# Kernel optimization log

Measured on AMD Instinct MI355X. Metric: run time of the kernel, lower is better.

Reference implementation:

```python
import jax, jax.numpy as jnp
import numpy as np

HEADS = 4
EPS_LN = 1e-6
EPS_IN = 1e-5


def _ln(x, g, b):
    m = x.mean(-1, keepdims=True)
    v = ((x - m) ** 2).mean(-1, keepdims=True)
    return (x - m) / jnp.sqrt(v + EPS_LN) * g + b


def _inorm(s):
    # nn.InstanceNorm2d(1) (affine=False): normalize each (batch, channel=head)
    # slice over the last two (N, N) dims, biased variance, eps=1e-5.
    m = s.mean((-2, -1), keepdims=True)
    v = ((s - m) ** 2).mean((-2, -1), keepdims=True)
    return (s - m) / jnp.sqrt(v + EPS_IN)


def setup_inputs() -> dict:
    key = jax.random.key(0)
    ks = jax.random.split(key, 32)
    B, C, Hh = 8, 256, HEADS
    sc = 1.0 / np.sqrt(C)

    def n(k, shape, s):
        return jax.random.normal(k, shape, jnp.float32) * s

    return {
        "x": n(ks[0], (B, C, 6, 6, 6), 1.0),
        # global branch params
        "g_tok_w": n(ks[1], (C,), 0.05), "g_tok_b": jnp.zeros((C,), jnp.float32),
        "g_ln1_g": jnp.ones((C,), jnp.float32), "g_ln1_b": jnp.zeros((C,), jnp.float32),
        "g_wq": n(ks[2], (C, C * Hh), sc), "g_wk": n(ks[3], (C, C * Hh), sc),
        "g_wv": n(ks[4], (C, C * Hh), sc), "g_wo": n(ks[5], (C * Hh, C), sc),
        "g_ln2_g": jnp.ones((C,), jnp.float32), "g_ln2_b": jnp.zeros((C,), jnp.float32),
        "g_mo_w": n(ks[6], (C, C), sc), "g_mo_b": jnp.zeros((C,), jnp.float32),
        # local branch params
        "l_pw": n(ks[7], (8, 8), 0.35), "l_pb": jnp.zeros((8,), jnp.float32),
        "l_ln1_g": jnp.ones((C,), jnp.float32), "l_ln1_b": jnp.zeros((C,), jnp.float32),
        "l_wq": n(ks[8], (C, C * Hh), sc), "l_wk": n(ks[9], (C, C * Hh), sc),
        "l_wv": n(ks[10], (C, C * Hh), sc), "l_wo": n(ks[11], (C * Hh, C), sc),
        "l_ln2_g": jnp.ones((C,), jnp.float32), "l_ln2_b": jnp.zeros((C,), jnp.float32),
        "l_mo_w": n(ks[12], (C, C), sc), "l_mo_b": jnp.zeros((C,), jnp.float32),
    }


def _global_branch(x, tok_w, tok_b, ln1_g, ln1_b, wq, wk, wv, wo, ln2_g, ln2_b, mo_w, mo_b):
    B, C, D, H, W = x.shape
    Hh = HEADS
    # TokenLearner_Global: conv1x1x1 (1->256) then mean over (D,H,W), then
    # view(B,C,C).mean(dim=1).  Since the conv is 1x1 on a single input channel,
    # this collapses exactly to: w * mean(x over C,D,H,W) + b.
    m = x.mean((1, 2, 3, 4))                       # (B,)
    tok = m[:, None] * tok_w + tok_b               # (B, C)
    res = tok
    t = _ln(tok, ln1_g, ln1_b)                     # (B, C)
    q = (t @ wq).reshape(B, Hh, C)                 # heads outer in the 1024 split
    k = (t @ wk).reshape(B, Hh, C)
    v = (t @ wv).reshape(B, Hh, C)
    # mh_q^T (B,h,C,1) @ mh_k (B,h,1,C) -> rank-1 (B,h,C,C) score map
    score = q[:, :, :, None] * k[:, :, None, :]
    a = jax.nn.softmax(_inorm(score), axis=-1)
    o = jnp.einsum('bhij,bhj->bhi', a, v)          # attn @ mh_v^T -> (B,h,C)
    # permute(0,3,2,1).view: flatten as (c, heads) with c outer
    o = o.transpose(0, 2, 1).reshape(B, C * Hh)
    out = o @ wo                                   # (B, C)
    tok2 = _ln(out + res, ln2_g, ln2_b)            # (B, C)
    # map_out conv1x1 + GELU on a spatially-constant expand -> compute once
    g = jax.nn.gelu(jnp.einsum('bc,oc->bo', tok2, mo_w) + mo_b, approximate=False)
    return jnp.broadcast_to(g[:, :, None, None, None], (B, C, D, H, W))


def _local_branch(x, pw, pb, ln1_g, ln1_b, wq, wk, wv, wo, ln2_g, ln2_b, mo_w, mo_b):
    B, C, D, H, W = x.shape
    Hh = HEADS
    # TokenLearner_Local: conv3d(1->8, k=2, s=2) per channel == patchify 2x2x2
    xp = x.reshape(B * C, 3, 2, 3, 2, 3, 2).transpose(0, 1, 3, 5, 2, 4, 6)
    xp = xp.reshape(B * C, 27, 8)                  # (BC, patches, patch_vol)
    tok = xp @ pw.T + pb                           # (BC, 27, 8) embed_dim=8
    tok = tok.reshape(B, C, 3, 3, 3, 2, 2, 2)
    # res: (b c)(d h w)(p1 p2 p3) -> b (d p1 h p2 w p3) c
    res = tok.transpose(0, 2, 5, 3, 6, 4, 7, 1).reshape(B, 216, C)
    # attn input: (b c)(d h w)(p1 p2 p3) -> (b d h w) (p1 p2 p3) c
    e = tok.reshape(B, C, 3, 3, 3, 8).transpose(0, 2, 3, 4, 5, 1).reshape(B * 27, 8, C)
    e = _ln(e, ln1_g, ln1_b)
    # (c heads) split: c outer, heads inner
    q = (e @ wq).reshape(B * 27, 8, C, Hh).transpose(0, 3, 2, 1)   # (B27,h,C,8)
    k = (e @ wk).reshape(B * 27, 8, C, Hh).transpose(0, 3, 1, 2)   # (B27,h,8,C)
    v = (e @ wv).reshape(B * 27, 8, C, Hh).transpose(0, 3, 2, 1)   # (B27,h,C,8)
    score = q @ k                                                  # (B27,h,C,C)
    a = jax.nn.softmax(_inorm(score), axis=-1)
    o = a @ v                                                      # (B27,h,C,8)
    # (b d h w) heads c (p1 p2 p3) -> b (d p1 h p2 w p3) (c heads)
    o = o.reshape(B, 3, 3, 3, Hh, C, 2, 2, 2)
    o = o.transpose(0, 1, 6, 2, 7, 3, 8, 5, 4).reshape(B, 216, C * Hh)
    out = o @ wo                                                   # (B,216,C)
    t2 = _ln(out + res, ln2_g, ln2_b)
    xm = t2.transpose(0, 2, 1).reshape(B, C, D, H, W)
    return jax.nn.gelu(
        jnp.einsum('bcdhw,oc->bodhw', xm, mo_w) + mo_b[None, :, None, None, None],
        approximate=False)


def reference(x,
              g_tok_w, g_tok_b, g_ln1_g, g_ln1_b, g_wq, g_wk, g_wv, g_wo,
              g_ln2_g, g_ln2_b, g_mo_w, g_mo_b,
              l_pw, l_pb, l_ln1_g, l_ln1_b, l_wq, l_wk, l_wv, l_wo,
              l_ln2_g, l_ln2_b, l_mo_w, l_mo_b):
    g = _global_branch(x, g_tok_w, g_tok_b, g_ln1_g, g_ln1_b, g_wq, g_wk, g_wv,
                       g_wo, g_ln2_g, g_ln2_b, g_mo_w, g_mo_b)
    l = _local_branch(x, l_pw, l_pb, l_ln1_g, l_ln1_b, l_wq, l_wk, l_wv,
                      l_wo, l_ln2_g, l_ln2_b, l_mo_w, l_mo_b)
    return x + g + l
```

## Files before the change

### kernel.cpp

```cpp
#include <hip/hip_runtime.h>
#include <stdint.h>
#include <math.h>

#define DEVFN __device__ __forceinline__
typedef unsigned short u16;
typedef short bf16x8 __attribute__((ext_vector_type(8)));
typedef float f32x4  __attribute__((ext_vector_type(4)));

DEVFN float blk_sum(float v, float* s4) {
  #pragma unroll
  for (int o = 32; o > 0; o >>= 1) v += __shfl_down(v, o, 64);
  __syncthreads();
  if ((threadIdx.x & 63) == 0) s4[threadIdx.x >> 6] = v;
  __syncthreads();
  return s4[0] + s4[1] + s4[2] + s4[3];
}

DEVFN void blk_sum2(float a, float b, float* out, float (*s)[4]) {
  #pragma unroll
  for (int o = 32; o > 0; o >>= 1) {
    a += __shfl_down(a, o, 64);
    b += __shfl_down(b, o, 64);
  }
  __syncthreads();
  if ((threadIdx.x & 63) == 0) {
    int wi = threadIdx.x >> 6;
    s[0][wi] = a; s[1][wi] = b;
  }
  __syncthreads();
  out[0] = s[0][0] + s[0][1] + s[0][2] + s[0][3];
  out[1] = s[1][0] + s[1][1] + s[1][2] + s[1][3];
}

DEVFN void blk_sum17(float* v, float (*s)[4]) {
  #pragma unroll
  for (int o = 32; o > 0; o >>= 1)
    #pragma unroll
    for (int i = 0; i < 17; ++i) v[i] += __shfl_down(v[i], o, 64);
  __syncthreads();
  if ((threadIdx.x & 63) == 0) {
    int wi = threadIdx.x >> 6;
    #pragma unroll
    for (int i = 0; i < 17; ++i) s[i][wi] = v[i];
  }
  __syncthreads();
  #pragma unroll
  for (int i = 0; i < 17; ++i) v[i] = s[i][0] + s[i][1] + s[i][2] + s[i][3];
}

DEVFN float gelu_f(float x) {
  return 0.5f * x * (1.f + erff(x * 0.7071067811865475f));
}

DEVFN u16 bf16_rne(float f) {
  uint32_t u = __float_as_uint(f);
  return (u16)((u + 0x7fffu + ((u >> 16) & 1u)) >> 16);
}

DEVFN float bf2f(u16 v) { return __uint_as_float(((uint32_t)v) << 16); }

DEVFN void gload16(const u16* g, u16* l) {
  auto gp = (const __attribute__((address_space(1))) uint32_t*)(uintptr_t)g;
  auto lp = (__attribute__((address_space(3))) uint32_t*)(uintptr_t)l;
  __builtin_amdgcn_global_load_lds(gp, lp, 16, 0, 0);
}

DEVFN void stage64x256(const u16* G, size_t gstride, u16* L, int w, int lane) {
  #pragma unroll
  for (int i = 0; i < 8; ++i) {
    int row = w * 16 + 2 * i + (lane >> 5);
    int c16 = (lane & 31) ^ (row & 7);
    gload16(G + (size_t)row * gstride + c16 * 8, L + (w * 16 + 2 * i) * 256);
  }
}
DEVFN bf16x8 lread(const u16* L, int row, int k16) {
  return *(const bf16x8*)&L[row * 256 + ((k16 ^ (row & 7)) << 3)];
}

DEVFN void trc_tile(const float* __restrict__ in, u16* __restrict__ out,
                    int R, int C, int r0, int c0, float (*tile)[33], int tid) {
  int tx = tid & 31, ty = tid >> 5;
  for (int i = ty; i < 32; i += 8) tile[i][tx] = in[(size_t)(r0 + i) * C + c0 + tx];
  __syncthreads();
  for (int i = ty; i < 32; i += 8)
    out[(size_t)(c0 + i) * R + r0 + tx] = bf16_rne(tile[tx][i]);
}

__global__ __launch_bounds__(256) void k_l_tok_prep(
    const float* __restrict__ x, const float* __restrict__ pw,
    const float* __restrict__ pb, const float* __restrict__ g1,
    const float* __restrict__ b1, float* __restrict__ res,
    u16* __restrict__ eln_bf, float* __restrict__ g_part,
    const float* __restrict__ wq, const float* __restrict__ wk,
    const float* __restrict__ wv, const float* __restrict__ wo,
    const float* __restrict__ mow, u16* __restrict__ WcatT,
    u16* __restrict__ woT, u16* __restrict__ moB) {
  __shared__ __align__(16) char smem[8448];
  int bid0 = blockIdx.x, tid = threadIdx.x;
  if (bid0 < 216) {
    float* pws = (float*)smem;
    float (*s17)[4] = (float(*)[4])(smem + 256);
    int b = bid0 / 27, patch = bid0 % 27;
    int pz = patch / 9, py = (patch / 3) % 3, px = patch % 3;
    int c = tid;
    if (c < 64) pws[c] = pw[c];
    __syncthreads();
    const float* xb = x + (size_t)(b * 256 + c) * 216 + (2 * pz) * 36 + (2 * py) * 6 + 2 * px;
    float2 t00 = *(const float2*)&xb[0],  t01 = *(const float2*)&xb[6];
    float2 t10 = *(const float2*)&xb[36], t11 = *(const float2*)&xb[42];
    float xv[8] = {t00.x, t00.y, t01.x, t01.y, t10.x, t10.y, t11.x, t11.y};
    float v[8];
    #pragma unroll
    for (int p = 0; p < 8; ++p) {
      float a = pb[p];
      #pragma unroll
      for (int j = 0; j < 8; ++j) a = fmaf(xv[j], pws[p * 8 + j], a);
      v[p] = a;
    }
    float sums[17];
    sums[0] = xv[0] + xv[1] + xv[2] + xv[3] + xv[4] + xv[5] + xv[6] + xv[7];
    #pragma unroll
    for (int p = 0; p < 8; ++p) { sums[1 + p] = v[p]; sums[9 + p] = v[p] * v[p]; }
    blk_sum17(sums, s17);
    if (c == 0) g_part[bid0] = sums[0];
    float gg = g1[c], bb = b1[c];
    #pragma unroll
    for (int p = 0; p < 8; ++p) {
      int sz = 2 * pz + (p >> 2), sy = 2 * py + ((p >> 1) & 1), sx = 2 * px + (p & 1);
      int t = b * 216 + sz * 36 + sy * 6 + sx;
      float mu = sums[1 + p] * (1.f / 256.f);
      float var = sums[9 + p] * (1.f / 256.f) - mu * mu;
      res[t * 256 + c] = v[p];
      eln_bf[t * 256 + c] = bf16_rne((v[p] - mu) * rsqrtf(var + 1e-6f) * gg + bb);
    }
  } else {
    float (*tile)[33] = (float(*)[33])smem;
    int bid = bid0 - 216;
    if (bid < 768) {
      int which = bid >> 8, b2 = bid & 255;
      const float* in = (which == 0) ? wq : (which == 1) ? wk : wv;
      u16* out = WcatT + which * 262144;
      int r0 = (b2 & 7) * 32, c0 = (b2 >> 3) * 32;
      trc_tile(in, out, 256, 1024, r0, c0, tile, tid);
    } else if (bid < 1024) {
      int b2 = bid - 768;
      int r0 = (b2 & 31) * 32, c0 = (b2 >> 5) * 32;
      trc_tile(wo, woT, 1024, 256, r0, c0, tile, tid);
    } else {
      int i = (bid - 1024) * 256 + tid;
      moB[i] = bf16_rne(mow[i]);
    }
  }
}

__global__ __launch_bounds__(256) void k_gemm_qkv_fused(
    const u16* __restrict__ A, const u16* __restrict__ BT, u16* __restrict__ C,
    const float* __restrict__ g_part, const float* __restrict__ tw_,
    const float* __restrict__ tb_, const float* __restrict__ g1,
    const float* __restrict__ b1, const float* __restrict__ wq,
    const float* __restrict__ wk, const float* __restrict__ wv,
    float* __restrict__ gqkv) {
  __shared__ __align__(16) char smem[65536];
  int bid = blockIdx.x, tid = threadIdx.x;
  if (bid < 48) {
    float* ts = (float*)smem;
    float (*red)[4][8] = (float(*)[4][8])(smem + 8192);
    float* s4 = (float*)(smem + 16384);
    float* m_s = (float*)(smem + 16400);
    float tw = tw_[tid], tb = tb_[tid], gg = g1[tid], bb = b1[tid];
    float S1 = blk_sum(tw, s4);
    float S2 = blk_sum(tw * tw, s4);
    float S3 = blk_sum(tb, s4);
    float S4 = blk_sum(tb * tb, s4);
    float S5 = blk_sum(tw * tb, s4);
    {
      int b = tid >> 5, sl = tid & 31;
      float a = (sl < 27) ? g_part[b * 27 + sl] : 0.f;
      #pragma unroll
      for (int o = 16; o > 0; o >>= 1) a += __shfl_down(a, o, 32);
      if (sl == 0) m_s[b] = a * (1.f / 55296.f);
    }
    __syncthreads();
    #pragma unroll
    for (int b = 0; b < 8; ++b) {
      float m = m_s[b];
      float mu = (m * S1 + S3) * (1.f / 256.f);
      float var = (m * m * S2 + 2.f * m * S5 + S4) * (1.f / 256.f) - mu * mu;
      ts[b * 256 + tid] = (m * tw + tb - mu) * rsqrtf(var + 1e-6f) * gg + bb;
    }
    __syncthreads();
    int col0 = bid * 64;
    int cl = tid & 63, kq = tid >> 6;
    int col = col0 + cl;
    int m = col >> 10, cc = col & 1023;
    const float* W = (m == 0) ? wq : (m == 1) ? wk : wv;
    float acc[8] = {};
    for (int c0 = kq * 64; c0 < kq * 64 + 64; c0 += 8) {
      float wbuf[8];
      #pragma unroll
      for (int j = 0; j < 8; ++j) wbuf[j] = W[(c0 + j) * 1024 + cc];
      #pragma unroll
      for (int j = 0; j < 8; ++j) {
        float w = wbuf[j];
        #pragma unroll
        for (int b = 0; b < 8; ++b) acc[b] = fmaf(ts[b * 256 + c0 + j], w, acc[b]);
      }
    }
    #pragma unroll
    for (int b = 0; b < 8; ++b) red[cl][kq][b] = acc[b];
    __syncthreads();
    if (kq == 0) {
      #pragma unroll
      for (int b = 0; b < 8; ++b)
        gqkv[b * 3072 + col] = red[cl][0][b] + red[cl][1][b] + red[cl][2][b] + red[cl][3][b];
    }
  } else {
    const int N = 3072, K = 256;
    u16* aL = (u16*)smem;
    u16* bL = (u16*)smem + 16384;
    int t0 = bid - 48;
    int tile = (t0 & 7) * 162 + (t0 >> 3);
    int rowblk = (tile % 27) * 64, colblk = (tile / 27) * 64;
    int lane = tid & 63, w = tid >> 6;
    int wr = (w >> 1) * 32, wc = (w & 1) * 32;
    int fm = lane & 15, lg = lane >> 4;
    #pragma unroll
    for (int i = 0; i < 8; ++i) {
      int c16 = w * 8 + i;
      gload16(&A[(size_t)(rowblk + lane) * K + c16 * 8], aL + c16 * 512);
      gload16(&BT[(size_t)(colblk + lane) * K + c16 * 8], bL + c16 * 512);
    }
    __syncthreads();
    f32x4 acc[2][2] = {};
    #pragma unroll
    for (int kk = 0; kk < 8; ++kk) {
      int k16 = kk * 4 + lg;
      bf16x8 bn0 = *(const bf16x8*)&bL[k16 * 512 + (wc + fm) * 8];
      bf16x8 bn1 = *(const bf16x8*)&bL[k16 * 512 + (wc + 16 + fm) * 8];
      bf16x8 af0 = *(const bf16x8*)&aL[k16 * 512 + (wr + fm) * 8];
      bf16x8 af1 = *(const bf16x8*)&aL[k16 * 512 + (wr + 16 + fm) * 8];
      acc[0][0] = __builtin_amdgcn_mfma_f32_16x16x32_bf16(af0, bn0, acc[0][0], 0, 0, 0);
      acc[0][1] = __builtin_amdgcn_mfma_f32_16x16x32_bf16(af0, bn1, acc[0][1], 0, 0, 0);
      acc[1][0] = __builtin_amdgcn_mfma_f32_16x16x32_bf16(af1, bn0, acc[1][0], 0, 0, 0);
      acc[1][1] = __builtin_amdgcn_mfma_f32_16x16x32_bf16(af1, bn1, acc[1][1], 0, 0, 0);
    }
    __syncthreads();
    u16* ct = aL;
    #pragma unroll
    for (int mi = 0; mi < 2; ++mi)
      #pragma unroll
      for (int ni = 0; ni < 2; ++ni)
        #pragma unroll
        for (int r = 0; r < 4; ++r)
          ct[(wr + mi * 16 + lg * 4 + r) * 72 + wc + ni * 16 + fm] = bf16_rne(acc[mi][ni][r]);
    __syncthreads();
    #pragma unroll
    for (int pass = 0; pass < 2; ++pass) {
      int id = pass * 256 + tid;
      int r = id >> 3, u = id & 7;
      *(uint4*)&C[(size_t)(rowblk + r) * N + colblk + u * 8] = *(uint4*)&ct[r * 72 + u * 8];
    }
  }
}

__global__ __launch_bounds__(256) void k_l_attn_fused(
    const u16* __restrict__ qkv, u16* __restrict__ o_buf,
    const float* __restrict__ gq, float* __restrict__ g_o) {
  __shared__ __align__(16) uint4 Qb[256], Kb[256];
  __shared__ __align__(16) u16 vt[16][264];
  __shared__ __align__(16) u16 Pl[256][72];
  __shared__ float rqA[64][4], rkA[64][4], rlq[64][4], rlk[64][4], s_ab[2];
  int bid = blockIdx.x, tid = threadIdx.x;
  if (bid < 32) {
    float* ks = (float*)Qb;
    float* vs = ks + 256;
    float* s4 = (float*)Kb;
    int b = bid >> 2, h = bid & 3;
    int i = tid;
    const float* base = gq + b * 3072 + h * 256;
    float q = base[i];
    float k = base[1024 + i];
    ks[i] = k;
    vs[i] = base[2048 + i];
    float sq  = blk_sum(q, s4);
    float sq2 = blk_sum(q * q, s4);
    float sk  = blk_sum(k, s4);
    float sk2 = blk_sum(k * k, s4);
    float tot  = sq * sk * (1.f / 65536.f);
    float tot2 = sq2 * sk2 * (1.f / 65536.f);
    float rstd = rsqrtf(tot2 - tot * tot + 1e-5f);
    float A = rstd, B = -tot * rstd;
    float den = 0.f, num = 0.f;
    for (int j = 0; j < 256; ++j) {
      float w = __expf(fmaf(q * ks[j], A, B));
      den += w; num += w * vs[j];
    }
    g_o[b * 1024 + (i << 2) + h] = num / den;
    return;
  }
  int nb = bid - 32;
  int n = nb >> 2, h = nb & 3;
  int b = n / 27, patch = n % 27;
  int bz = 2 * (patch / 9), by = 2 * ((patch / 3) % 3), bx = 2 * (patch % 3);
  {
    int c = tid;
    u16 qv[8], kv[8], vv[8];
    #pragma unroll
    for (int p = 0; p < 8; ++p) {
      int t_l = b * 216 + (bz + (p >> 2)) * 36 + (by + ((p >> 1) & 1)) * 6 + (bx + (p & 1));
      const u16* row = qkv + (size_t)t_l * 3072 + (c << 2) + h;
      qv[p] = row[0]; kv[p] = row[1024]; vv[p] = row[2048];
    }
    uint32_t qw[4], kw[4];
    #pragma unroll
    for (int i = 0; i < 4; ++i) {
      qw[i] = (uint32_t)qv[2 * i] | ((uint32_t)qv[2 * i + 1] << 16);
      kw[i] = (uint32_t)kv[2 * i] | ((uint32_t)kv[2 * i + 1] << 16);
    }
    Qb[c] = make_uint4(qw[0], qw[1], qw[2], qw[3]);
    Kb[c] = make_uint4(kw[0], kw[1], kw[2], kw[3]);
    #pragma unroll
    for (int p = 0; p < 8; ++p) vt[p][c] = vv[p];
    vt[8][c] = 0x3F80u;
    #pragma unroll
    for (int r2 = 9; r2 < 16; ++r2) vt[r2][c] = 0;
  }
  __syncthreads();
  {
    int p = tid & 63, chunk = tid >> 6;
    int d = p >> 3, e = p & 7;
    float aq = 0.f, ak = 0.f, lq = 0.f, lk = 0.f;
    for (int cc = chunk * 64; cc < chunk * 64 + 64; ++cc) {
      const u16* qr = (const u16*)&Qb[cc];
      const u16* kr = (const u16*)&Kb[cc];
      float qd = bf2f(qr[d]), qe = bf2f(qr[e]);
      float kd = bf2f(kr[d]), ke = bf2f(kr[e]);
      aq = fmaf(qd, qe, aq); ak = fmaf(kd, ke, ak);
      if (e == 0) { lq += qd; lk += kd; }
    }
    rqA[p][chunk] = aq; rkA[p][chunk] = ak; rlq[p][chunk] = lq; rlk[p][chunk] = lk;
    __syncthreads();
    if (tid < 64) {
      float gq2 = rqA[tid][0] + rqA[tid][1] + rqA[tid][2] + rqA[tid][3];
      float gk = rkA[tid][0] + rkA[tid][1] + rkA[tid][2] + rkA[tid][3];
      float vprod = gq2 * gk, vmu = 0.f;
      if ((tid & 7) == 0) {
        float slq = rlq[tid][0] + rlq[tid][1] + rlq[tid][2] + rlq[tid][3];
        float slk = rlk[tid][0] + rlk[tid][1] + rlk[tid][2] + rlk[tid][3];
        vmu = slq * slk;
      }
      #pragma unroll
      for (int o = 32; o > 0; o >>= 1) {
        vprod += __shfl_down(vprod, o, 64);
        vmu   += __shfl_down(vmu, o, 64);
      }
      if (tid == 0) {
        float mu = vmu * (1.f / 65536.f), m2 = vprod * (1.f / 65536.f);
        float rstd = rsqrtf(m2 - mu * mu + 1e-5f);
        s_ab[0] = rstd; s_ab[1] = -mu * rstd;
      }
    }
    __syncthreads();
  }
  float Af = s_ab[0], Bf = s_ab[1];
  int lane = tid & 63, w = tid >> 6;
  int l15 = lane & 15, lg = lane >> 4;
  bf16x8 qf[4];
  #pragma unroll
  for (int qt = 0; qt < 4; ++qt)
    qf[qt] = *(const bf16x8*)&Qb[w * 64 + qt * 16 + l15];
  f32x4 acc_o[4] = {};
  #pragma unroll 1
  for (int jc = 0; jc < 4; ++jc) {
    bf16x8 kf[4];
    #pragma unroll
    for (int jt = 0; jt < 4; ++jt) {
      bf16x8 z = {};
      if (lg == 0) z = *(const bf16x8*)&Kb[jc * 64 + jt * 16 + l15];
      kf[jt] = z;
    }
    #pragma unroll
    for (int jt = 0; jt < 4; ++jt) {
      #pragma unroll
      for (int qt = 0; qt < 4; ++qt) {
        f32x4 zc = {};
        f32x4 s = __builtin_amdgcn_mfma_f32_16x16x32_bf16(kf[jt], qf[qt], zc, 0, 0, 0);
        float e0 = __expf(fmaf(s[0], Af, Bf));
        float e1 = __expf(fmaf(s[1], Af, Bf));
        float e2 = __expf(fmaf(s[2], Af, Bf));
        float e3 = __expf(fmaf(s[3], Af, Bf));
        uint32_t w0 = (__float_as_uint(e0) >> 16) | (__float_as_uint(e1) & 0xFFFF0000u);
        uint32_t w1 = (__float_as_uint(e2) >> 16) | (__float_as_uint(e3) & 0xFFFF0000u);
        int q = w * 64 + qt * 16 + l15;
        *(uint2*)&Pl[q][jt * 16 + lg * 4] = make_uint2(w0, w1);
      }
    }
    #pragma unroll
    for (int ks2 = 0; ks2 < 2; ++ks2) {
      bf16x8 vf = *(const bf16x8*)&vt[l15][jc * 64 + ks2 * 32 + lg * 8];
      #pragma unroll
      for (int qt = 0; qt < 4; ++qt) {
        bf16x8 pf = *(const bf16x8*)&Pl[w * 64 + qt * 16 + l15][ks2 * 32 + lg * 8];
        acc_o[qt] = __builtin_amdgcn_mfma_f32_16x16x32_bf16(pf, vf, acc_o[qt], 0, 0, 0);
      }
    }
  }
  int src = ((lane & 48) + 8) << 2;
  int p = l15;
  int t_l = b * 216 + (bz + (p >> 2)) * 36 + (by + ((p >> 1) & 1)) * 6 + (bx + (p & 1));
  #pragma unroll
  for (int qt = 0; qt < 4; ++qt) {
    #pragma unroll
    for (int r = 0; r < 4; ++r) {
      float den = __int_as_float(__builtin_amdgcn_ds_bpermute(src, __float_as_int(acc_o[qt][r])));
      if (p < 8) {
        int q = w * 64 + qt * 16 + lg * 4 + r;
        o_buf[(size_t)t_l * 1024 + (q << 2) + h] = bf16_rne(acc_o[qt][r] / den);
      }
    }
  }
}

__global__ __launch_bounds__(256) void k_gemm_sk_fused(
    const u16* __restrict__ A, const u16* __restrict__ BT, float* __restrict__ Cp,
    const float* __restrict__ g_o, const float* __restrict__ wo,
    float* __restrict__ part) {
  __shared__ __align__(16) char smem[65536];
  int bid = blockIdx.x, tid = threadIdx.x;
  if (bid < 32) {
    float* os = (float*)smem;
    int kc = bid;
    os[tid] = g_o[(tid >> 5) * 1024 + kc * 32 + (tid & 31)];
    __syncthreads();
    float acc[8] = {};
    #pragma unroll
    for (int kk = 0; kk < 32; ++kk) {
      float w = wo[(size_t)(kc * 32 + kk) * 256 + tid];
      #pragma unroll
      for (int b = 0; b < 8; ++b) acc[b] = fmaf(os[b * 32 + kk], w, acc[b]);
    }
    #pragma unroll
    for (int b = 0; b < 8; ++b) part[kc * 2048 + b * 256 + tid] = acc[b];
  } else {
    const int M = 1728, N = 256, K = 1024;
    u16* aL = (u16*)smem;
    u16* bL = (u16*)smem + 16384;
    int bid2 = bid - 32;
    int rowblk = (bid2 % 27) * 64, colblk = ((bid2 / 27) & 3) * 64;
    int kz = bid2 / 108;
    float* C = Cp + (size_t)kz * M * N;
    int lane = tid & 63, w = tid >> 6;
    int wr = (w >> 1) * 32, wc = (w & 1) * 32;
    int fm = lane & 15, lg = lane >> 4;
    f32x4 acc[2][2] = {};
    #pragma unroll 1
    for (int step = 0; step < 2; ++step) {
      int kt = kz * 512 + step * 256;
      __syncthreads();
      stage64x256(A + (size_t)rowblk * K + kt, K, aL, w, lane);
      stage64x256(BT + (size_t)colblk * K + kt, K, bL, w, lane);
      __syncthreads();
      #pragma unroll
      for (int kk = 0; kk < 8; ++kk) {
        int k16 = kk * 4 + lg;
        bf16x8 bn0 = lread(bL, wc + fm, k16);
        bf16x8 bn1 = lread(bL, wc + 16 + fm, k16);
        bf16x8 af0 = lread(aL, wr + fm, k16);
        bf16x8 af1 = lread(aL, wr + 16 + fm, k16);
        acc[0][0] = __builtin_amdgcn_mfma_f32_16x16x32_bf16(af0, bn0, acc[0][0], 0, 0, 0);
        acc[0][1] = __builtin_amdgcn_mfma_f32_16x16x32_bf16(af0, bn1, acc[0][1], 0, 0, 0);
        acc[1][0] = __builtin_amdgcn_mfma_f32_16x16x32_bf16(af1, bn0, acc[1][0], 0, 0, 0);
        acc[1][1] = __builtin_amdgcn_mfma_f32_16x16x32_bf16(af1, bn1, acc[1][1], 0, 0, 0);
      }
    }
    __syncthreads();
    float* ct = (float*)smem;
    #pragma unroll
    for (int mi = 0; mi < 2; ++mi)
      #pragma unroll
      for (int ni = 0; ni < 2; ++ni)
        #pragma unroll
        for (int r = 0; r < 4; ++r)
          ct[(wr + mi * 16 + lg * 4 + r) * 64 + wc + ni * 16 + fm] = acc[mi][ni][r];
    __syncthreads();
    #pragma unroll
    for (int pass = 0; pass < 4; ++pass) {
      int id = pass * 256 + tid;
      int r = id >> 4, u = id & 15;
      *(float4*)&C[(size_t)(rowblk + r) * N + colblk + u * 4] = *(float4*)&ct[r * 64 + u * 4];
    }
  }
}

__global__ __launch_bounds__(256) void k_l_ln2_fused(
    const float* __restrict__ proj0, const float* __restrict__ proj1,
    const float* __restrict__ res, const float* __restrict__ g2,
    const float* __restrict__ b2, u16* __restrict__ t2b,
    const float* __restrict__ part, const float* __restrict__ g_part,
    const float* __restrict__ tw_, const float* __restrict__ tb_,
    const float* __restrict__ gg2, const float* __restrict__ gb2,
    float* __restrict__ t2g) {
  __shared__ float s2v[2][4];
  int bid = blockIdx.x, c = threadIdx.x;
  if (bid < 8) {
    int b = bid;
    float a = (c < 27) ? g_part[b * 27 + c] : 0.f;
    float m = blk_sum(a, (float*)s2v) * (1.f / 55296.f);
    float v = m * tw_[c] + tb_[c];
    #pragma unroll
    for (int kc = 0; kc < 32; ++kc) v += part[kc * 2048 + b * 256 + c];
    float r2[2];
    blk_sum2(v, v * v, r2, s2v);
    float mu = r2[0] * (1.f / 256.f);
    float var = r2[1] * (1.f / 256.f) - mu * mu;
    t2g[b * 256 + c] = (v - mu) * rsqrtf(var + 1e-6f) * gg2[c] + gb2[c];
  } else {
    int t = bid - 8;
    float v = proj0[t * 256 + c] + proj1[t * 256 + c] + res[t * 256 + c];
    float r2[2];
    blk_sum2(v, v * v, r2, s2v);
    float mu = r2[0] * (1.f / 256.f);
    float var = r2[1] * (1.f / 256.f) - mu * mu;
    t2b[t * 256 + c] = bf16_rne((v - mu) * rsqrtf(var + 1e-6f) * g2[c] + b2[c]);
  }
}

__global__ __launch_bounds__(256) void k_g_mo(
    const float* __restrict__ t2g, const float* __restrict__ mow,
    const float* __restrict__ mob, float* __restrict__ g_vec) {
  __shared__ float ts[2048];
  int tid = threadIdx.x;
  for (int i = tid; i < 2048; i += 256) ts[i] = t2g[i];
  __syncthreads();
  int ol = tid >> 5, cs = tid & 31;
  int o = blockIdx.x * 8 + ol;
  const float* wrow = mow + (size_t)o * 256;
  float acc[8] = {};
  #pragma unroll
  for (int i = 0; i < 8; ++i) {
    float w = wrow[i * 32 + cs];
    #pragma unroll
    for (int b = 0; b < 8; ++b) acc[b] = fmaf(ts[b * 256 + i * 32 + cs], w, acc[b]);
  }
  #pragma unroll
  for (int b = 0; b < 8; ++b) {
    float v = acc[b];
    #pragma unroll
    for (int off = 16; off > 0; off >>= 1) v += __shfl_down(v, off, 32);
    if (cs == 0) g_vec[b * 256 + o] = gelu_f(v + mob[o]);
  }
}

__global__ __launch_bounds__(256) void k_gemm_mo_final(
    const u16* __restrict__ A, const u16* __restrict__ BT,
    const float* __restrict__ x, const float* __restrict__ gvec,
    const float* __restrict__ mob, float* __restrict__ out) {
  __shared__ __align__(16) char smem[65536];
  u16* aL = (u16*)smem;
  u16* bL = (u16*)smem + 16384;
  float (*ct)[65] = (float(*)[65])smem;
  const int K = 256;
  int tid = threadIdx.x;
  int rowblk = blockIdx.x * 64, colblk = blockIdx.y * 64;
  int lane = tid & 63, w = tid >> 6;
  int wr = (w >> 1) * 32, wc = (w & 1) * 32;
  int fm = lane & 15, lg = lane >> 4;
  stage64x256(A + (size_t)rowblk * K, K, aL, w, lane);
  stage64x256(BT + (size_t)colblk * K, K, bL, w, lane);
  __syncthreads();
  f32x4 acc[2][2] = {};
  #pragma unroll
  for (int kk = 0; kk < 8; ++kk) {
    int k16 = kk * 4 + lg;
    bf16x8 bn0 = lread(bL, wc + fm, k16);
    bf16x8 bn1 = lread(bL, wc + 16 + fm, k16);
    bf16x8 af0 = lread(aL, wr + fm, k16);
    bf16x8 af1 = lread(aL, wr + 16 + fm, k16);
    acc[0][0] = __builtin_amdgcn_mfma_f32_16x16x32_bf16(af0, bn0, acc[0][0], 0, 0, 0);
    acc[0][1] = __builtin_amdgcn_mfma_f32_16x16x32_bf16(af0, bn1, acc[0][1], 0, 0, 0);
    acc[1][0] = __builtin_amdgcn_mfma_f32_16x16x32_bf16(af1, bn0, acc[1][0], 0, 0, 0);
    acc[1][1] = __builtin_amdgcn_mfma_f32_16x16x32_bf16(af1, bn1, acc[1][1], 0, 0, 0);
  }
  __syncthreads();
  int row_l0 = wr + lg * 4;
  #pragma unroll
  for (int mi = 0; mi < 2; ++mi)
    #pragma unroll
    for (int ni = 0; ni < 2; ++ni)
      #pragma unroll
      for (int r = 0; r < 4; ++r)
        ct[row_l0 + mi * 16 + r][wc + ni * 16 + fm] = acc[mi][ni][r];
  __syncthreads();
  int s_l = tid & 63;
  #pragma unroll 4
  for (int pass = 0; pass < 16; ++pass) {
    int col_l = (tid >> 6) * 16 + pass;
    int row = rowblk + s_l, col = colblk + col_l;
    int b = row / 216, s = row - b * 216;
    size_t idx = (size_t)b * 55296 + (size_t)col * 216 + s;
    out[idx] = x[idx] + gvec[b * 256 + col] + gelu_f(ct[s_l][col_l] + mob[col]);
  }
}

extern "C" void kernel_launch(void* const* d_in, const int* in_sizes, int n_in,
                              void* d_out, int out_size, void* d_ws, size_t ws_size,
                              hipStream_t stream) {
  const float* x     = (const float*)d_in[0];
  const float* g_tw  = (const float*)d_in[1];
  const float* g_tb  = (const float*)d_in[2];
  const float* g_l1g = (const float*)d_in[3];
  const float* g_l1b = (const float*)d_in[4];
  const float* g_wq  = (const float*)d_in[5];
  const float* g_wk  = (const float*)d_in[6];
  const float* g_wv  = (const float*)d_in[7];
  const float* g_wo  = (const float*)d_in[8];
  const float* g_l2g = (const float*)d_in[9];
  const float* g_l2b = (const float*)d_in[10];
  const float* g_mow = (const float*)d_in[11];
  const float* g_mob = (const float*)d_in[12];
  const float* l_pw  = (const float*)d_in[13];
  const float* l_pb  = (const float*)d_in[14];
  const float* l_l1g = (const float*)d_in[15];
  const float* l_l1b = (const float*)d_in[16];
  const float* l_wq  = (const float*)d_in[17];
  const float* l_wk  = (const float*)d_in[18];
  const float* l_wv  = (const float*)d_in[19];
  const float* l_wo  = (const float*)d_in[20];
  const float* l_l2g = (const float*)d_in[21];
  const float* l_l2b = (const float*)d_in[22];
  const float* l_mow = (const float*)d_in[23];
  const float* l_mob = (const float*)d_in[24];
  float* out = (float*)d_out;
  float* ws  = (float*)d_ws;

  float* g_qkv  = ws + 4096;
  float* g_o    = ws + 28672;
  float* g_vec  = ws + 36864;
  float* g_part = ws + 38912;
  float* res    = ws + 40960;
  u16*   eln_bf = (u16*)(ws + 483328);
  u16*   WcatT  = (u16*)(ws + 704512);
  u16*   woT    = (u16*)(ws + 1097728);
  u16*   moB    = (u16*)(ws + 1228800);
  u16*   qkvb   = (u16*)(ws + 1261568);
  u16*   o_buf  = (u16*)(ws + 6569984);
  float* proj   = ws + 7454720;
  u16*   t2b    = (u16*)(ws + 8339456);
  float* part_wo= ws + 8560640;
  float* t2g    = ws + 8626176;

  k_l_tok_prep<<<1496, 256, 0, stream>>>(x, l_pw, l_pb, l_l1g, l_l1b,
                                         res, eln_bf, g_part,
                                         l_wq, l_wk, l_wv, l_wo, l_mow,
                                         WcatT, woT, moB);
  k_gemm_qkv_fused<<<1344, 256, 0, stream>>>(eln_bf, WcatT, qkvb,
                                             g_part, g_tw, g_tb, g_l1g, g_l1b,
                                             g_wq, g_wk, g_wv, g_qkv);
  k_l_attn_fused<<<896, 256, 0, stream>>>(qkvb, o_buf, g_qkv, g_o);
  k_gemm_sk_fused<<<248, 256, 0, stream>>>(o_buf, woT, proj, g_o, g_wo, part_wo);
  k_l_ln2_fused<<<1736, 256, 0, stream>>>(proj, proj + 442368, res,
                                          l_l2g, l_l2b, t2b,
                                          part_wo, g_part, g_tw, g_tb,
                                          g_l2g, g_l2b, t2g);
  k_g_mo<<<32, 256, 0, stream>>>(t2g, g_mow, g_mob, g_vec);
  k_gemm_mo_final<<<dim3(27, 4), 256, 0, stream>>>(t2b, moB, x, g_vec, l_mob, out);
}
```

Measured before the change: 91.32 us.

## Fuse global MLP-out matvec into LN2 kernel and use column-major LDS staging

Removes the separate k_g_mo launch by computing the global branch's mo_w matvec and GELU inside the first 8 blocks of the LN2 kernel. Each thread reads its own weight row, which is strided and uncoalesced across the block. Separately, GEMM LDS staging changes from a row-major XOR-swizzled layout to a k-chunk-major layout, unified through a new stageCM helper. The aim is to cut one kernel launch and simplify LDS addressing, at the cost of possibly slower weight loads and different LDS bank behaviour.

```diff
diff --git a/kernel.cpp b/kernel.cpp
--- a/kernel.cpp
+++ b/kernel.cpp
@@ -65,16 +65,12 @@
   __builtin_amdgcn_global_load_lds(gp, lp, 16, 0, 0);
 }
 
-DEVFN void stage64x256(const u16* G, size_t gstride, u16* L, int w, int lane) {
+DEVFN void stageCM(const u16* G, size_t gstride, u16* L, int w, int lane) {
   #pragma unroll
   for (int i = 0; i < 8; ++i) {
-    int row = w * 16 + 2 * i + (lane >> 5);
-    int c16 = (lane & 31) ^ (row & 7);
-    gload16(G + (size_t)row * gstride + c16 * 8, L + (w * 16 + 2 * i) * 256);
-  }
-}
-DEVFN bf16x8 lread(const u16* L, int row, int k16) {
-  return *(const bf16x8*)&L[row * 256 + ((k16 ^ (row & 7)) << 3)];
+    int c16 = w * 8 + i;
+    gload16(G + (size_t)lane * gstride + c16 * 8, L + c16 * 512);
+  }
 }
 
 DEVFN void trc_tile(const float* __restrict__ in, u16* __restrict__ out,
@@ -224,12 +220,8 @@
     int lane = tid & 63, w = tid >> 6;
     int wr = (w >> 1) * 32, wc = (w & 1) * 32;
     int fm = lane & 15, lg = lane >> 4;
-    #pragma unroll
-    for (int i = 0; i < 8; ++i) {
-      int c16 = w * 8 + i;
-      gload16(&A[(size_t)(rowblk + lane) * K + c16 * 8], aL + c16 * 512);
-      gload16(&BT[(size_t)(colblk + lane) * K + c16 * 8], bL + c16 * 512);
-    }
+    stageCM(A + (size_t)rowblk * K, K, aL, w, lane);
+    stageCM(BT + (size_t)colblk * K, K, bL, w, lane);
     __syncthreads();
     f32x4 acc[2][2] = {};
     #pragma unroll
@@ -457,16 +449,16 @@
     for (int step = 0; step < 2; ++step) {
       int kt = kz * 512 + step * 256;
       __syncthreads();
-      stage64x256(A + (size_t)rowblk * K + kt, K, aL, w, lane);
-      stage64x256(BT + (size_t)colblk * K + kt, K, bL, w, lane);
+      stageCM(A + (size_t)rowblk * K + kt, K, aL, w, lane);
+      stageCM(BT + (size_t)colblk * K + kt, K, bL, w, lane);
       __syncthreads();
       #pragma unroll
       for (int kk = 0; kk < 8; ++kk) {
         int k16 = kk * 4 + lg;
-        bf16x8 bn0 = lread(bL, wc + fm, k16);
-        bf16x8 bn1 = lread(bL, wc + 16 + fm, k16);
-        bf16x8 af0 = lread(aL, wr + fm, k16);
-        bf16x8 af1 = lread(aL, wr + 16 + fm, k16);
+        bf16x8 bn0 = *(const bf16x8*)&bL[k16 * 512 + (wc + fm) * 8];
+        bf16x8 bn1 = *(const bf16x8*)&bL[k16 * 512 + (wc + 16 + fm) * 8];
+        bf16x8 af0 = *(const bf16x8*)&aL[k16 * 512 + (wr + fm) * 8];
+        bf16x8 af1 = *(const bf16x8*)&aL[k16 * 512 + (wr + 16 + fm) * 8];
         acc[0][0] = __builtin_amdgcn_mfma_f32_16x16x32_bf16(af0, bn0, acc[0][0], 0, 0, 0);
         acc[0][1] = __builtin_amdgcn_mfma_f32_16x16x32_bf16(af0, bn1, acc[0][1], 0, 0, 0);
         acc[1][0] = __builtin_amdgcn_mfma_f32_16x16x32_bf16(af1, bn0, acc[1][0], 0, 0, 0);
@@ -499,8 +491,10 @@
     const float* __restrict__ part, const float* __restrict__ g_part,
     const float* __restrict__ tw_, const float* __restrict__ tb_,
     const float* __restrict__ gg2, const float* __restrict__ gb2,
-    float* __restrict__ t2g) {
+    const float* __restrict__ mow, const float* __restrict__ mob,
+    float* __restrict__ g_vec) {
   __shared__ float s2v[2][4];
+  __shared__ float ts[256];
   int bid = blockIdx.x, c = threadIdx.x;
   if (bid < 8) {
     int b = bid;
@@ -513,7 +507,18 @@
     blk_sum2(v, v * v, r2, s2v);
     float mu = r2[0] * (1.f / 256.f);
     float var = r2[1] * (1.f / 256.f) - mu * mu;
-    t2g[b * 256 + c] = (v - mu) * rsqrtf(var + 1e-6f) * gg2[c] + gb2[c];
+    ts[c] = (v - mu) * rsqrtf(var + 1e-6f) * gg2[c] + gb2[c];
+    __syncthreads();
+    float a2 = mob[c];
+    const float* wrow = mow + (size_t)c * 256;
+    for (int c0 = 0; c0 < 256; c0 += 8) {
+      float wbuf[8];
+      #pragma unroll
+      for (int j = 0; j < 8; ++j) wbuf[j] = wrow[c0 + j];
+      #pragma unroll
+      for (int j = 0; j < 8; ++j) a2 = fmaf(ts[c0 + j], wbuf[j], a2);
+    }
+    g_vec[b * 256 + c] = gelu_f(a2);
   } else {
     int t = bid - 8;
     float v = proj0[t * 256 + c] + proj1[t * 256 + c] + res[t * 256 + c];
@@ -522,32 +527,6 @@
     float mu = r2[0] * (1.f / 256.f);
     float var = r2[1] * (1.f / 256.f) - mu * mu;
     t2b[t * 256 + c] = bf16_rne((v - mu) * rsqrtf(var + 1e-6f) * g2[c] + b2[c]);
-  }
-}
-
-__global__ __launch_bounds__(256) void k_g_mo(
-    const float* __restrict__ t2g, const float* __restrict__ mow,
-    const float* __restrict__ mob, float* __restrict__ g_vec) {
-  __shared__ float ts[2048];
-  int tid = threadIdx.x;
-  for (int i = tid; i < 2048; i += 256) ts[i] = t2g[i];
-  __syncthreads();
-  int ol = tid >> 5, cs = tid & 31;
-  int o = blockIdx.x * 8 + ol;
-  const float* wrow = mow + (size_t)o * 256;
-  float acc[8] = {};
-  #pragma unroll
-  for (int i = 0; i < 8; ++i) {
-    float w = wrow[i * 32 + cs];
-    #pragma unroll
-    for (int b = 0; b < 8; ++b) acc[b] = fmaf(ts[b * 256 + i * 32 + cs], w, acc[b]);
-  }
-  #pragma unroll
-  for (int b = 0; b < 8; ++b) {
-    float v = acc[b];
-    #pragma unroll
-    for (int off = 16; off > 0; off >>= 1) v += __shfl_down(v, off, 32);
-    if (cs == 0) g_vec[b * 256 + o] = gelu_f(v + mob[o]);
   }
 }
 
@@ -565,17 +544,17 @@
   int lane = tid & 63, w = tid >> 6;
   int wr = (w >> 1) * 32, wc = (w & 1) * 32;
   int fm = lane & 15, lg = lane >> 4;
-  stage64x256(A + (size_t)rowblk * K, K, aL, w, lane);
-  stage64x256(BT + (size_t)colblk * K, K, bL, w, lane);
+  stageCM(A + (size_t)rowblk * K, K, aL, w, lane);
+  stageCM(BT + (size_t)colblk * K, K, bL, w, lane);
   __syncthreads();
   f32x4 acc[2][2] = {};
   #pragma unroll
   for (int kk = 0; kk < 8; ++kk) {
     int k16 = kk * 4 + lg;
-    bf16x8 bn0 = lread(bL, wc + fm, k16);
-    bf16x8 bn1 = lread(bL, wc + 16 + fm, k16);
-    bf16x8 af0 = lread(aL, wr + fm, k16);
-    bf16x8 af1 = lread(aL, wr + 16 + fm, k16);
+    bf16x8 bn0 = *(const bf16x8*)&bL[k16 * 512 + (wc + fm) * 8];
+    bf16x8 bn1 = *(const bf16x8*)&bL[k16 * 512 + (wc + 16 + fm) * 8];
+    bf16x8 af0 = *(const bf16x8*)&aL[k16 * 512 + (wr + fm) * 8];
+    bf16x8 af1 = *(const bf16x8*)&aL[k16 * 512 + (wr + 16 + fm) * 8];
     acc[0][0] = __builtin_amdgcn_mfma_f32_16x16x32_bf16(af0, bn0, acc[0][0], 0, 0, 0);
     acc[0][1] = __builtin_amdgcn_mfma_f32_16x16x32_bf16(af0, bn1, acc[0][1], 0, 0, 0);
     acc[1][0] = __builtin_amdgcn_mfma_f32_16x16x32_bf16(af1, bn0, acc[1][0], 0, 0, 0);
@@ -647,7 +626,6 @@
   float* proj   = ws + 7454720;
   u16*   t2b    = (u16*)(ws + 8339456);
   float* part_wo= ws + 8560640;
-  float* t2g    = ws + 8626176;
 
   k_l_tok_prep<<<1496, 256, 0, stream>>>(x, l_pw, l_pb, l_l1g, l_l1b,
                                          res, eln_bf, g_part,
@@ -661,7 +639,6 @@
   k_l_ln2_fused<<<1736, 256, 0, stream>>>(proj, proj + 442368, res,
                                           l_l2g, l_l2b, t2b,
                                           part_wo, g_part, g_tw, g_tb,
-                                          g_l2g, g_l2b, t2g);
-  k_g_mo<<<32, 256, 0, stream>>>(t2g, g_mow, g_mob, g_vec);
+                                          g_l2g, g_l2b, g_mow, g_mob, g_vec);
   k_gemm_mo_final<<<dim3(27, 4), 256, 0, stream>>>(t2b, moB, x, g_vec, l_mob, out);
 }
```

Result: slower. 93.66 us (+2.6%).
